# Kernel tuning notes

Hardware: AMD Instinct MI355X
Metric: run time of the kernel (lower is better)

The kernel has to match this reference:

```python
import jax, jax.numpy as jnp
import numpy as np


def setup_inputs() -> dict:
    key = jax.random.key(0)
    ks = jax.random.split(key, 8)
    B, T, U, D, H, V = 4, 128, 64, 512, 640, 1024
    return {
        "source_encodings": jax.random.normal(ks[0], (B, T, D), dtype=jnp.float32),
        "source_lengths": jax.random.randint(ks[1], (B,), 1, T + 1).astype(jnp.int32),
        "target_encodings": jax.random.normal(ks[2], (B, U, D), dtype=jnp.float32),
        "target_lengths": jax.random.randint(ks[3], (B,), 1, U + 1).astype(jnp.int32),
        "W1": jax.random.normal(ks[4], (2 * D, H), dtype=jnp.float32) * (1.0 / np.sqrt(2 * D)),
        "b1": jax.random.normal(ks[5], (H,), dtype=jnp.float32) * 0.01,
        "W2": jax.random.normal(ks[6], (H, V), dtype=jnp.float32) * (1.0 / np.sqrt(H)),
        "b2": jax.random.normal(ks[7], (V,), dtype=jnp.float32) * 0.01,
    }


def reference(source_encodings, source_lengths, target_encodings, target_lengths, W1, b1, W2, b2):
    # CONCAT combination: Linear(concat(s, t)) == s @ W1[:D] + t @ W1[D:] + b1.
    # This avoids materializing the [B,T,U,2D] expand+concat tensor while
    # computing identical math to the original torch module.
    D = source_encodings.shape[-1]
    W1s, W1t = W1[:D], W1[D:]
    ps = jnp.einsum("btd,dh->bth", source_encodings, W1s)   # [B,T,H]
    pt = jnp.einsum("bud,dh->buh", target_encodings, W1t)   # [B,U,H]
    h = jnp.tanh(ps[:, :, None, :] + pt[:, None, :, :] + b1)  # [B,T,U,H]
    logits = jnp.einsum("btuh,hv->btuv", h, W2) + b2          # [B,T,U,V]
    # Module is in eval mode (not self.training) -> log_softmax applied.
    out = jax.nn.log_softmax(logits, axis=-1)
    return (out, source_lengths, target_lengths)
```

## Files before the change

### kernel.cpp

```cpp
#include <hip/hip_runtime.h>
#include <hip/hip_bf16.h>

#define B_ 4
#define T_ 128
#define U_ 64
#define D_ 512
#define H_ 640
#define V_ 1024

typedef float f32x4 __attribute__((ext_vector_type(4)));
typedef __bf16 bf16x8 __attribute__((ext_vector_type(8)));

union U4BF8 { uint4 u; bf16x8 v; };

__device__ __forceinline__ unsigned short f2bf(float x) {
  union { float f; unsigned int u; } a; a.f = x;
  unsigned int r = a.u + 0x7FFFu + ((a.u >> 16) & 1u);
  return (unsigned short)(r >> 16);
}

__global__ void k_pack_w2(const float* __restrict__ W2, uint4* __restrict__ w2p,
                          const int* __restrict__ slen, const int* __restrict__ tlen,
                          float* __restrict__ out_tail) {
  int kq = blockIdx.x;
  int tid = threadIdx.x;
  for (int i = 0; i < 4; ++i) {
    int n = tid + i * 256;
    float f[8];
    #pragma unroll
    for (int j = 0; j < 8; ++j) f[j] = W2[(size_t)(kq * 8 + j) * V_ + n];
    unsigned int w[4];
    #pragma unroll
    for (int j = 0; j < 4; ++j)
      w[j] = (unsigned)f2bf(f[2 * j]) | ((unsigned)f2bf(f[2 * j + 1]) << 16);
    uint4 p; p.x = w[0]; p.y = w[1]; p.z = w[2]; p.w = w[3];
    w2p[kq * V_ + n] = p;
  }
  if (blockIdx.x == 0 && tid < 8)
    out_tail[tid] = (tid < 4) ? (float)slen[tid] : (float)tlen[tid - 4];
}

__global__ __launch_bounds__(640) void k_proj(
    const float* __restrict__ src, const float* __restrict__ tgt,
    const float* __restrict__ W1, const float* __restrict__ b1,
    float* __restrict__ ps, float* __restrict__ pt) {
  __shared__ __align__(16) float lin[D_ * 4];
  int bid = blockIdx.x, tid = threadIdx.x;
  bool is_t = bid >= 128;
  const float* in; const float* w; float* outp;
  if (!is_t) {
    int r0 = bid * 4;
    in = src + (size_t)r0 * D_; w = W1; outp = ps + (size_t)r0 * H_;
  } else {
    int r0 = (bid - 128) * 4;
    in = tgt + (size_t)r0 * D_; w = W1 + (size_t)D_ * H_; outp = pt + (size_t)r0 * H_;
  }
  for (int idx = tid; idx < 4 * D_; idx += 640) {
    int r = idx >> 9, k = idx & (D_ - 1);
    lin[k * 4 + r] = in[idx];
  }
  __syncthreads();
  float a0 = 0.f, a1 = 0.f, a2 = 0.f, a3 = 0.f;
  int j = tid;
  for (int k = 0; k < D_; ++k) {
    float wv = w[(size_t)k * H_ + j];
    f32x4 x = *(const f32x4*)&lin[k * 4];
    a0 += x[0] * wv; a1 += x[1] * wv; a2 += x[2] * wv; a3 += x[3] * wv;
  }
  float bb = is_t ? b1[j] : 0.f;
  outp[0 * H_ + j] = a0 + bb;
  outp[1 * H_ + j] = a1 + bb;
  outp[2 * H_ + j] = a2 + bb;
  outp[3 * H_ + j] = a3 + bb;
}

__global__ __launch_bounds__(1024, 4) void k_joint(
    const float* __restrict__ ps, const float* __restrict__ pt,
    const uint4* __restrict__ w2p, const float* __restrict__ b2,
    float* __restrict__ out) {
  __shared__ uint4 ldsA[80 * 64];
  __shared__ float red[64][16][2];
  __shared__ float lzs[64];
  int bid = blockIdx.x;
  int b = bid >> 7, t = bid & 127;
  int tid = threadIdx.x;
  const float* psrow = ps + (size_t)(b * T_ + t) * H_;
  const float* ptb   = pt + (size_t)(b * U_) * H_;

  for (int c = tid; c < 80 * 64; c += 1024) {
    int m = c / 80, kq = c - m * 80;
    const float4* pp = (const float4*)(psrow + kq * 8);
    const float4* qq = (const float4*)(ptb + (size_t)m * H_ + kq * 8);
    float4 p0 = pp[0], p1 = pp[1];
    float4 q0 = qq[0], q1 = qq[1];
    float x[8] = {p0.x + q0.x, p0.y + q0.y, p0.z + q0.z, p0.w + q0.w,
                  p1.x + q1.x, p1.y + q1.y, p1.z + q1.z, p1.w + q1.w};
    unsigned int wv[4];
    #pragma unroll
    for (int j = 0; j < 4; ++j) {
      float e0 = __expf(2.f * x[2 * j]);
      float h0 = 1.f - 2.f * __builtin_amdgcn_rcpf(e0 + 1.f);
      float e1 = __expf(2.f * x[2 * j + 1]);
      float h1 = 1.f - 2.f * __builtin_amdgcn_rcpf(e1 + 1.f);
      wv[j] = (unsigned)f2bf(h0) | ((unsigned)f2bf(h1) << 16);
    }
    uint4 pk; pk.x = wv[0]; pk.y = wv[1]; pk.z = wv[2]; pk.w = wv[3];
    ldsA[m * 80 + (kq ^ (m & 7))] = pk;
  }
  __syncthreads();

  int lane = tid & 63, wid = tid >> 6;
  int l16 = lane & 15, lg = lane >> 4;
  int xs = l16 & 7;

  f32x4 acc[4][4];
  #pragma unroll
  for (int mf = 0; mf < 4; ++mf)
    #pragma unroll
    for (int nf = 0; nf < 4; ++nf) {
      f32x4 z = {0.f, 0.f, 0.f, 0.f};
      acc[mf][nf] = z;
    }

  for (int kq0 = 0; kq0 < 80; kq0 += 4) {
    int kq = kq0 + lg;
    int kqx = kq ^ xs;
    U4BF8 a[4];
    #pragma unroll
    for (int mf = 0; mf < 4; ++mf)
      a[mf].u = ldsA[(mf * 16 + l16) * 80 + kqx];
    const uint4* bp = w2p + (size_t)kq * 1024 + wid * 64 + l16;
    #pragma unroll
    for (int nf = 0; nf < 4; ++nf) {
      U4BF8 bb; bb.u = bp[nf * 16];
      #pragma unroll
      for (int mf = 0; mf < 4; ++mf)
        acc[mf][nf] = __builtin_amdgcn_mfma_f32_16x16x32_bf16(
            a[mf].v, bb.v, acc[mf][nf], 0, 0, 0);
    }
  }

  {
    float b2v[4];
    #pragma unroll
    for (int nf = 0; nf < 4; ++nf) b2v[nf] = b2[wid * 64 + nf * 16 + l16];
    #pragma unroll
    for (int mf = 0; mf < 4; ++mf)
      #pragma unroll
      for (int nf = 0; nf < 4; ++nf)
        #pragma unroll
        for (int r = 0; r < 4; ++r)
          acc[mf][nf][r] += b2v[nf];
  }

  #pragma unroll
  for (int mf = 0; mf < 4; ++mf)
    #pragma unroll
    for (int r = 0; r < 4; ++r) {
      float pm = -3.4e38f;
      #pragma unroll
      for (int nf = 0; nf < 4; ++nf) pm = fmaxf(pm, acc[mf][nf][r]);
      pm = fmaxf(pm, __shfl_xor(pm, 1));
      pm = fmaxf(pm, __shfl_xor(pm, 2));
      pm = fmaxf(pm, __shfl_xor(pm, 4));
      pm = fmaxf(pm, __shfl_xor(pm, 8));
      float s = 0.f;
      #pragma unroll
      for (int nf = 0; nf < 4; ++nf) s += __expf(acc[mf][nf][r] - pm);
      s += __shfl_xor(s, 1);
      s += __shfl_xor(s, 2);
      s += __shfl_xor(s, 4);
      s += __shfl_xor(s, 8);
      if (l16 == 0) {
        int row = mf * 16 + lg * 4 + r;
        red[row][wid][0] = pm;
        red[row][wid][1] = s;
      }
    }
  __syncthreads();

  if (tid < 64) {
    float M = -3.4e38f;
    #pragma unroll
    for (int w16 = 0; w16 < 16; ++w16) M = fmaxf(M, red[tid][w16][0]);
    float S = 0.f;
    #pragma unroll
    for (int w16 = 0; w16 < 16; ++w16)
      S += red[tid][w16][1] * __expf(red[tid][w16][0] - M);
    lzs[tid] = M + __logf(S);
  }
  __syncthreads();

  float* outb = out + (size_t)(b * T_ + t) * U_ * V_;
  #pragma unroll
  for (int mf = 0; mf < 4; ++mf)
    #pragma unroll
    for (int r = 0; r < 4; ++r) {
      int row = mf * 16 + lg * 4 + r;
      float lz = lzs[row];
      float* orow = outb + (size_t)row * V_ + wid * 64 + l16;
      #pragma unroll
      for (int nf = 0; nf < 4; ++nf)
        orow[nf * 16] = acc[mf][nf][r] - lz;
    }
}

extern "C" void kernel_launch(void* const* d_in, const int* in_sizes, int n_in,
                              void* d_out, int out_size, void* d_ws, size_t ws_size,
                              hipStream_t stream) {
  const float* src = (const float*)d_in[0];
  const int*   slen = (const int*)d_in[1];
  const float* tgt = (const float*)d_in[2];
  const int*   tlen = (const int*)d_in[3];
  const float* W1 = (const float*)d_in[4];
  const float* b1 = (const float*)d_in[5];
  const float* W2 = (const float*)d_in[6];
  const float* b2 = (const float*)d_in[7];
  float* out = (float*)d_out;

  float* ps  = (float*)d_ws;
  float* pt  = ps + 512 * 640;
  uint4* w2p = (uint4*)(pt + 256 * 640);

  k_pack_w2<<<80, 256, 0, stream>>>(W2, w2p, slen, tlen,
                                    out + (size_t)B_ * T_ * U_ * V_);
  k_proj<<<192, 640, 0, stream>>>(src, tgt, W1, b1, ps, pt);
  k_joint<<<512, 1024, 0, stream>>>(ps, pt, w2p, b2, out);
}
```

Before: 109.4 us.

## Merge prep kernels, process two time steps per joint block, prefetch W2, vectorize stores

New measurement: 378.4 us. +246.0%, slower.

```diff
diff --git a/kernel.cpp b/kernel.cpp
--- a/kernel.cpp
+++ b/kernel.cpp
@@ -19,59 +19,59 @@
   return (unsigned short)(r >> 16);
 }
 
-__global__ void k_pack_w2(const float* __restrict__ W2, uint4* __restrict__ w2p,
-                          const int* __restrict__ slen, const int* __restrict__ tlen,
-                          float* __restrict__ out_tail) {
-  int kq = blockIdx.x;
-  int tid = threadIdx.x;
-  for (int i = 0; i < 4; ++i) {
-    int n = tid + i * 256;
-    float f[8];
-    #pragma unroll
-    for (int j = 0; j < 8; ++j) f[j] = W2[(size_t)(kq * 8 + j) * V_ + n];
-    unsigned int w[4];
-    #pragma unroll
-    for (int j = 0; j < 4; ++j)
-      w[j] = (unsigned)f2bf(f[2 * j]) | ((unsigned)f2bf(f[2 * j + 1]) << 16);
-    uint4 p; p.x = w[0]; p.y = w[1]; p.z = w[2]; p.w = w[3];
-    w2p[kq * V_ + n] = p;
-  }
-  if (blockIdx.x == 0 && tid < 8)
-    out_tail[tid] = (tid < 4) ? (float)slen[tid] : (float)tlen[tid - 4];
-}
-
-__global__ __launch_bounds__(640) void k_proj(
+__global__ __launch_bounds__(640) void k_prep(
+    const float* __restrict__ W2, uint4* __restrict__ w2p,
+    const int* __restrict__ slen, const int* __restrict__ tlen,
+    float* __restrict__ out_tail,
     const float* __restrict__ src, const float* __restrict__ tgt,
     const float* __restrict__ W1, const float* __restrict__ b1,
     float* __restrict__ ps, float* __restrict__ pt) {
   __shared__ __align__(16) float lin[D_ * 4];
   int bid = blockIdx.x, tid = threadIdx.x;
-  bool is_t = bid >= 128;
-  const float* in; const float* w; float* outp;
-  if (!is_t) {
-    int r0 = bid * 4;
-    in = src + (size_t)r0 * D_; w = W1; outp = ps + (size_t)r0 * H_;
+  if (bid < 192) {
+    bool is_t = bid >= 128;
+    const float* in; const float* w; float* outp;
+    if (!is_t) {
+      int r0 = bid * 4;
+      in = src + (size_t)r0 * D_; w = W1; outp = ps + (size_t)r0 * H_;
+    } else {
+      int r0 = (bid - 128) * 4;
+      in = tgt + (size_t)r0 * D_; w = W1 + (size_t)D_ * H_; outp = pt + (size_t)r0 * H_;
+    }
+    for (int idx = tid; idx < 4 * D_; idx += 640) {
+      int r = idx >> 9, k = idx & (D_ - 1);
+      lin[k * 4 + r] = in[idx];
+    }
+    __syncthreads();
+    float a0 = 0.f, a1 = 0.f, a2 = 0.f, a3 = 0.f;
+    int j = tid;
+    for (int k = 0; k < D_; ++k) {
+      float wv = w[(size_t)k * H_ + j];
+      f32x4 x = *(const f32x4*)&lin[k * 4];
+      a0 += x[0] * wv; a1 += x[1] * wv; a2 += x[2] * wv; a3 += x[3] * wv;
+    }
+    float bb = is_t ? b1[j] : 0.f;
+    outp[0 * H_ + j] = a0 + bb;
+    outp[1 * H_ + j] = a1 + bb;
+    outp[2 * H_ + j] = a2 + bb;
+    outp[3 * H_ + j] = a3 + bb;
   } else {
-    int r0 = (bid - 128) * 4;
-    in = tgt + (size_t)r0 * D_; w = W1 + (size_t)D_ * H_; outp = pt + (size_t)r0 * H_;
+    int kq = bid - 192;
+    for (int n = tid; n < V_; n += 640) {
+      int src_n = (n & ~63) | ((n & 15) * 4) | ((n >> 4) & 3);
+      float f[8];
+      #pragma unroll
+      for (int j = 0; j < 8; ++j) f[j] = W2[(size_t)(kq * 8 + j) * V_ + src_n];
+      unsigned int w[4];
+      #pragma unroll
+      for (int j = 0; j < 4; ++j)
+        w[j] = (unsigned)f2bf(f[2 * j]) | ((unsigned)f2bf(f[2 * j + 1]) << 16);
+      uint4 p; p.x = w[0]; p.y = w[1]; p.z = w[2]; p.w = w[3];
+      w2p[(size_t)kq * V_ + n] = p;
+    }
+    if (bid == 192 && tid < 8)
+      out_tail[tid] = (tid < 4) ? (float)slen[tid] : (float)tlen[tid - 4];
   }
-  for (int idx = tid; idx < 4 * D_; idx += 640) {
-    int r = idx >> 9, k = idx & (D_ - 1);
-    lin[k * 4 + r] = in[idx];
-  }
-  __syncthreads();
-  float a0 = 0.f, a1 = 0.f, a2 = 0.f, a3 = 0.f;
-  int j = tid;
-  for (int k = 0; k < D_; ++k) {
-    float wv = w[(size_t)k * H_ + j];
-    f32x4 x = *(const f32x4*)&lin[k * 4];
-    a0 += x[0] * wv; a1 += x[1] * wv; a2 += x[2] * wv; a3 += x[3] * wv;
-  }
-  float bb = is_t ? b1[j] : 0.f;
-  outp[0 * H_ + j] = a0 + bb;
-  outp[1 * H_ + j] = a1 + bb;
-  outp[2 * H_ + j] = a2 + bb;
-  outp[3 * H_ + j] = a3 + bb;
 }
 
 __global__ __launch_bounds__(1024, 4) void k_joint(
@@ -79,71 +79,78 @@
     const uint4* __restrict__ w2p, const float* __restrict__ b2,
     float* __restrict__ out) {
   __shared__ uint4 ldsA[80 * 64];
-  __shared__ float red[64][16][2];
+  __shared__ float red[16][64][2];
   __shared__ float lzs[64];
   int bid = blockIdx.x;
-  int b = bid >> 7, t = bid & 127;
+  int b = bid >> 6, tb = bid & 63;
   int tid = threadIdx.x;
-  const float* psrow = ps + (size_t)(b * T_ + t) * H_;
-  const float* ptb   = pt + (size_t)(b * U_) * H_;
-
-  for (int c = tid; c < 80 * 64; c += 1024) {
-    int m = c / 80, kq = c - m * 80;
-    const float4* pp = (const float4*)(psrow + kq * 8);
-    const float4* qq = (const float4*)(ptb + (size_t)m * H_ + kq * 8);
-    float4 p0 = pp[0], p1 = pp[1];
-    float4 q0 = qq[0], q1 = qq[1];
-    float x[8] = {p0.x + q0.x, p0.y + q0.y, p0.z + q0.z, p0.w + q0.w,
-                  p1.x + q1.x, p1.y + q1.y, p1.z + q1.z, p1.w + q1.w};
-    unsigned int wv[4];
-    #pragma unroll
-    for (int j = 0; j < 4; ++j) {
-      float e0 = __expf(2.f * x[2 * j]);
-      float h0 = 1.f - 2.f * __builtin_amdgcn_rcpf(e0 + 1.f);
-      float e1 = __expf(2.f * x[2 * j + 1]);
-      float h1 = 1.f - 2.f * __builtin_amdgcn_rcpf(e1 + 1.f);
-      wv[j] = (unsigned)f2bf(h0) | ((unsigned)f2bf(h1) << 16);
-    }
-    uint4 pk; pk.x = wv[0]; pk.y = wv[1]; pk.z = wv[2]; pk.w = wv[3];
-    ldsA[m * 80 + (kq ^ (m & 7))] = pk;
-  }
-  __syncthreads();
-
   int lane = tid & 63, wid = tid >> 6;
   int l16 = lane & 15, lg = lane >> 4;
   int xs = l16 & 7;
-
-  f32x4 acc[4][4];
-  #pragma unroll
-  for (int mf = 0; mf < 4; ++mf)
-    #pragma unroll
-    for (int nf = 0; nf < 4; ++nf) {
-      f32x4 z = {0.f, 0.f, 0.f, 0.f};
-      acc[mf][nf] = z;
-    }
-
-  for (int kq0 = 0; kq0 < 80; kq0 += 4) {
-    int kq = kq0 + lg;
-    int kqx = kq ^ xs;
-    U4BF8 a[4];
-    #pragma unroll
-    for (int mf = 0; mf < 4; ++mf)
-      a[mf].u = ldsA[(mf * 16 + l16) * 80 + kqx];
-    const uint4* bp = w2p + (size_t)kq * 1024 + wid * 64 + l16;
-    #pragma unroll
-    for (int nf = 0; nf < 4; ++nf) {
-      U4BF8 bb; bb.u = bp[nf * 16];
+  const float* ptb = pt + (size_t)(b * U_) * H_;
+  float4 b2v = *(const float4*)&b2[wid * 64 + l16 * 4];
+
+  for (int ti = 0; ti < 2; ++ti) {
+    int t = tb * 2 + ti;
+    const float* psrow = ps + (size_t)(b * T_ + t) * H_;
+
+    for (int c = tid; c < 80 * 64; c += 1024) {
+      int m = c / 80, kq = c - m * 80;
+      const float4* pp = (const float4*)(psrow + kq * 8);
+      const float4* qq = (const float4*)(ptb + (size_t)m * H_ + kq * 8);
+      float4 p0 = pp[0], p1 = pp[1];
+      float4 q0 = qq[0], q1 = qq[1];
+      float x[8] = {p0.x + q0.x, p0.y + q0.y, p0.z + q0.z, p0.w + q0.w,
+                    p1.x + q1.x, p1.y + q1.y, p1.z + q1.z, p1.w + q1.w};
+      unsigned int wv[4];
+      #pragma unroll
+      for (int j = 0; j < 4; ++j) {
+        float e0 = __expf(2.f * x[2 * j]);
+        float h0 = 1.f - 2.f * __builtin_amdgcn_rcpf(e0 + 1.f);
+        float e1 = __expf(2.f * x[2 * j + 1]);
+        float h1 = 1.f - 2.f * __builtin_amdgcn_rcpf(e1 + 1.f);
+        wv[j] = (unsigned)f2bf(h0) | ((unsigned)f2bf(h1) << 16);
+      }
+      uint4 pk; pk.x = wv[0]; pk.y = wv[1]; pk.z = wv[2]; pk.w = wv[3];
+      ldsA[m * 80 + (kq ^ (m & 7))] = pk;
+    }
+    __syncthreads();
+
+    f32x4 acc[4][4];
+    #pragma unroll
+    for (int mf = 0; mf < 4; ++mf)
+      #pragma unroll
+      for (int nf = 0; nf < 4; ++nf) {
+        f32x4 z = {0.f, 0.f, 0.f, 0.f};
+        acc[mf][nf] = z;
+      }
+
+    const uint4* bp0 = w2p + wid * 64 + l16;
+    U4BF8 bcur[4], bnxt[4];
+    #pragma unroll
+    for (int nf = 0; nf < 4; ++nf) bcur[nf].u = bp0[(size_t)lg * V_ + nf * 16];
+    for (int kq0 = 0; kq0 < 80; kq0 += 4) {
+      int kq = kq0 + lg;
+      U4BF8 a[4];
       #pragma unroll
       for (int mf = 0; mf < 4; ++mf)
-        acc[mf][nf] = __builtin_amdgcn_mfma_f32_16x16x32_bf16(
-            a[mf].v, bb.v, acc[mf][nf], 0, 0, 0);
-    }
-  }
-
-  {
-    float b2v[4];
-    #pragma unroll
-    for (int nf = 0; nf < 4; ++nf) b2v[nf] = b2[wid * 64 + nf * 16 + l16];
+        a[mf].u = ldsA[(mf * 16 + l16) * 80 + (kq ^ xs)];
+      if (kq0 < 76) {
+        #pragma unroll
+        for (int nf = 0; nf < 4; ++nf)
+          bnxt[nf].u = bp0[(size_t)(kq + 4) * V_ + nf * 16];
+      }
+      #pragma unroll
+      for (int nf = 0; nf < 4; ++nf)
+        #pragma unroll
+        for (int mf = 0; mf < 4; ++mf)
+          acc[mf][nf] = __builtin_amdgcn_mfma_f32_16x16x32_bf16(
+              a[mf].v, bcur[nf].v, acc[mf][nf], 0, 0, 0);
+      #pragma unroll
+      for (int nf = 0; nf < 4; ++nf) bcur[nf] = bnxt[nf];
+    }
+    __syncthreads();
+
     #pragma unroll
     for (int mf = 0; mf < 4; ++mf)
       #pragma unroll
@@ -151,58 +158,60 @@
         #pragma unroll
         for (int r = 0; r < 4; ++r)
           acc[mf][nf][r] += b2v[nf];
+
+    #pragma unroll
+    for (int mf = 0; mf < 4; ++mf)
+      #pragma unroll
+      for (int r = 0; r < 4; ++r) {
+        float pm = -3.4e38f;
+        #pragma unroll
+        for (int nf = 0; nf < 4; ++nf) pm = fmaxf(pm, acc[mf][nf][r]);
+        pm = fmaxf(pm, __shfl_xor(pm, 1));
+        pm = fmaxf(pm, __shfl_xor(pm, 2));
+        pm = fmaxf(pm, __shfl_xor(pm, 4));
+        pm = fmaxf(pm, __shfl_xor(pm, 8));
+        float s = 0.f;
+        #pragma unroll
+        for (int nf = 0; nf < 4; ++nf) s += __expf(acc[mf][nf][r] - pm);
+        s += __shfl_xor(s, 1);
+        s += __shfl_xor(s, 2);
+        s += __shfl_xor(s, 4);
+        s += __shfl_xor(s, 8);
+        if (l16 == 0) {
+          int row = mf * 16 + lg * 4 + r;
+          red[wid][row][0] = pm;
+          red[wid][row][1] = s;
+        }
+      }
+    __syncthreads();
+
+    if (tid < 64) {
+      float M = -3.4e38f;
+      #pragma unroll
+      for (int w16 = 0; w16 < 16; ++w16) M = fmaxf(M, red[w16][tid][0]);
+      float S = 0.f;
+      #pragma unroll
+      for (int w16 = 0; w16 < 16; ++w16)
+        S += red[w16][tid][1] * __expf(red[w16][tid][0] - M);
+      lzs[tid] = M + __logf(S);
+    }
+    __syncthreads();
+
+    float* outb = out + (size_t)(b * T_ + t) * U_ * V_;
+    #pragma unroll
+    for (int mf = 0; mf < 4; ++mf)
+      #pragma unroll
+      for (int r = 0; r < 4; ++r) {
+        int row = mf * 16 + lg * 4 + r;
+        float lz = lzs[row];
+        float4 o;
+        o.x = acc[mf][0][r] - lz;
+        o.y = acc[mf][1][r] - lz;
+        o.z = acc[mf][2][r] - lz;
+        o.w = acc[mf][3][r] - lz;
+        *(float4*)&outb[(size_t)row * V_ + wid * 64 + l16 * 4] = o;
+      }
   }
-
-  #pragma unroll
-  for (int mf = 0; mf < 4; ++mf)
-    #pragma unroll
-    for (int r = 0; r < 4; ++r) {
-      float pm = -3.4e38f;
-      #pragma unroll
-      for (int nf = 0; nf < 4; ++nf) pm = fmaxf(pm, acc[mf][nf][r]);
-      pm = fmaxf(pm, __shfl_xor(pm, 1));
-      pm = fmaxf(pm, __shfl_xor(pm, 2));
-      pm = fmaxf(pm, __shfl_xor(pm, 4));
-      pm = fmaxf(pm, __shfl_xor(pm, 8));
-      float s = 0.f;
-      #pragma unroll
-      for (int nf = 0; nf < 4; ++nf) s += __expf(acc[mf][nf][r] - pm);
-      s += __shfl_xor(s, 1);
-      s += __shfl_xor(s, 2);
-      s += __shfl_xor(s, 4);
-      s += __shfl_xor(s, 8);
-      if (l16 == 0) {
-        int row = mf * 16 + lg * 4 + r;
-        red[row][wid][0] = pm;
-        red[row][wid][1] = s;
-      }
-    }
-  __syncthreads();
-
-  if (tid < 64) {
-    float M = -3.4e38f;
-    #pragma unroll
-    for (int w16 = 0; w16 < 16; ++w16) M = fmaxf(M, red[tid][w16][0]);
-    float S = 0.f;
-    #pragma unroll
-    for (int w16 = 0; w16 < 16; ++w16)
-      S += red[tid][w16][1] * __expf(red[tid][w16][0] - M);
-    lzs[tid] = M + __logf(S);
-  }
-  __syncthreads();
-
-  float* outb = out + (size_t)(b * T_ + t) * U_ * V_;
-  #pragma unroll
-  for (int mf = 0; mf < 4; ++mf)
-    #pragma unroll
-    for (int r = 0; r < 4; ++r) {
-      int row = mf * 16 + lg * 4 + r;
-      float lz = lzs[row];
-      float* orow = outb + (size_t)row * V_ + wid * 64 + l16;
-      #pragma unroll
-      for (int nf = 0; nf < 4; ++nf)
-        orow[nf * 16] = acc[mf][nf][r] - lz;
-    }
 }
 
 extern "C" void kernel_launch(void* const* d_in, const int* in_sizes, int n_in,
@@ -222,8 +231,8 @@
   float* pt  = ps + 512 * 640;
   uint4* w2p = (uint4*)(pt + 256 * 640);
 
-  k_pack_w2<<<80, 256, 0, stream>>>(W2, w2p, slen, tlen,
-                                    out + (size_t)B_ * T_ * U_ * V_);
-  k_proj<<<192, 640, 0, stream>>>(src, tgt, W1, b1, ps, pt);
-  k_joint<<<512, 1024, 0, stream>>>(ps, pt, w2p, b2, out);
-}
+  k_prep<<<272, 640, 0, stream>>>(W2, w2p, slen, tlen,
+                                  out + (size_t)B_ * T_ * U_ * V_,
+                                  src, tgt, W1, b1, ps, pt);
+  k_joint<<<256, 1024, 0, stream>>>(ps, pt, w2p, b2, out);
+}
```
